# Kernel optimization log

Measured on AMD Instinct MI355X. Metric: run time of the kernel, lower is better.

## Reference

```python
import jax, jax.numpy as jnp
import numpy as np

B, T, I, H, O = 8192, 1024, 7, 100, 1


def setup_inputs() -> dict:
    key = jax.random.key(0)
    ks = jax.random.split(key, 7)
    s = 1.0 / np.sqrt(H)  # PyTorch default init bound for RNN/Linear(H)
    return {
        "x": jax.random.normal(ks[0], (B, T, I), dtype=jnp.float32),
        "W_ih": jax.random.uniform(ks[1], (H, I), jnp.float32, -s, s),
        "W_hh": jax.random.uniform(ks[2], (H, H), jnp.float32, -s, s),
        "b_ih": jax.random.uniform(ks[3], (H,), jnp.float32, -s, s),
        "b_hh": jax.random.uniform(ks[4], (H,), jnp.float32, -s, s),
        "W_fc": jax.random.uniform(ks[5], (O, H), jnp.float32, -s, s),
        "b_fc": jax.random.uniform(ks[6], (O,), jnp.float32, -s, s),
    }


def reference(x, W_ih, W_hh, b_ih, b_hh, W_fc, b_fc):
    # Precompute the input projection for all timesteps in one GEMM:
    # x_proj[b,t,h] = x[b,t,:] @ W_ih^T + b_ih + b_hh  (both biases folded in)
    x_proj = jnp.einsum('bti,hi->bth', x, W_ih) + b_ih + b_hh  # [B,T,H]

    def step(h, xt):
        # h_t = relu(x_t W_ih^T + b_ih + h_{t-1} W_hh^T + b_hh)
        h_new = jax.nn.relu(xt + h @ W_hh.T)
        return h_new, None

    h0 = jnp.zeros((x.shape[0], W_hh.shape[0]), dtype=x.dtype)  # [B,H]
    hT, _ = jax.lax.scan(step, h0, jnp.swapaxes(x_proj, 0, 1))  # scan over T

    # fc applied to last timestep only: out[:, -1, :] @ W_fc^T + b_fc
    return hT @ W_fc.T + b_fc  # [B,O]
```

## Files before the change

### kernel.cpp

```cpp
#include <hip/hip_runtime.h>


typedef _Float16 half8 __attribute__((ext_vector_type(8)));
typedef _Float16 half4 __attribute__((ext_vector_type(4)));
typedef float f32x4 __attribute__((ext_vector_type(4)));
typedef unsigned u32x4 __attribute__((ext_vector_type(4)));
typedef unsigned u32x2 __attribute__((ext_vector_type(2)));

static __device__ __forceinline__ unsigned pkrtz(float a, float b) {
    return __builtin_bit_cast(unsigned, __builtin_amdgcn_cvt_pkrtz(a, b));
}
static __device__ __forceinline__ f32x4 ld4(const float* p) {
    typedef f32x4 __attribute__((aligned(4))) f32x4a;
    return *(const f32x4a*)p;
}
static __device__ __forceinline__ u32x2 relu_pack(const f32x4 a) {
    u32x2 u = { pkrtz(a[0], a[1]), pkrtz(a[2], a[3]) };
    half4 h = __builtin_bit_cast(half4, u);
    const half4 z = { (_Float16)0, (_Float16)0, (_Float16)0, (_Float16)0 };
    h = __builtin_elementwise_max(h, z);
    return __builtin_bit_cast(u32x2, h);
}

#define MFMA16(a, b, c) __builtin_amdgcn_mfma_f32_16x16x32_f16(a, b, c, 0, 0, 0)

template<int NT, int TI0, int WID>
static __device__ __forceinline__ void rnn_half(
    const int l, const int lm, const int q, const bool q1,
    const float* __restrict__ x,
    const float* __restrict__ W_ih, const float* __restrict__ W_hh,
    const float* __restrict__ b_ih, const float* __restrict__ b_hh,
    const float* __restrict__ W_fc, const float* __restrict__ b_fc,
    float* __restrict__ out,
    u32x2 (*xch)[2][4][64], float* red)
{
    half8 w[NT][4];
#pragma unroll
    for (int i = 0; i < NT; ++i) {
        const int np = 16 * (TI0 + i) + lm;
#pragma unroll
        for (int kt = 0; kt < 4; ++kt) {
            half8 hw;
#pragma unroll
            for (int jj = 0; jj < 8; ++jj) {
                float v = 0.f;
                if (np < 100) {
                    if (jj < 4) {
                        int p = 16 * kt + 4 * q + jj;
                        if (p < 100) v = W_hh[np * 100 + p];
                    } else if (kt < 3) {
                        int p = 16 * (kt + 4) + 4 * q + (jj - 4);
                        if (p < 100) v = W_hh[np * 100 + p];
                    } else {
                        if (q == 0)      v = W_ih[np * 7 + (jj - 4)];
                        else if (q == 1) v = (jj < 7) ? W_ih[np * 7 + jj]
                                             : (b_ih[np] + b_hh[np]);
                    }
                }
                hw[jj] = (_Float16)v;
            }
            w[i][kt] = hw;
        }
    }

    const float* xr = x + (size_t)(blockIdx.x * 16 + lm) * 7168;
    const int xo = q1 ? 3 : 0;

    const u32x4 zz = {0u, 0u, 0u, 0u};
    const half8 hz = __builtin_bit_cast(half8, zz);

    half8 hf[4];
    {
        f32x4 v = ld4(xr + xo);
        float x0 = q1 ? v.y : v.x, x1 = q1 ? v.z : v.y;
        float x2 = q1 ? v.w : v.z, x3 = q1 ? 1.0f : v.w;
        hf[0] = hz; hf[1] = hz; hf[2] = hz;
        u32x4 h3 = {0u, 0u, pkrtz(x0, x1), pkrtz(x2, x3)};
        hf[3] = __builtin_bit_cast(half8, h3);
    }

    f32x4 xv[4];
#pragma unroll
    for (int s = 1; s <= 4; ++s) xv[s & 3] = ld4(xr + s * 7 + xo);

    const f32x4 kZ = {0.f, 0.f, 0.f, 0.f};
    f32x4 acc[NT];
#pragma unroll
    for (int i = 0; i < NT; ++i) acc[i] = kZ;

    for (int tb = 0; tb < 1024; tb += 4) {
#pragma unroll
        for (int u = 0; u < 4; ++u) {
            const int t = tb + u;
            const int p = u & 1;

#pragma unroll
            for (int kt = 0; kt < 4; ++kt)
#pragma unroll
                for (int i = 0; i < NT; ++i)
                    acc[i] = MFMA16(w[i][kt], hf[kt], kt == 0 ? kZ : acc[i]);

            u32x2 own[NT];
#pragma unroll
            for (int i = 0; i < NT; ++i) {
                own[i] = relu_pack(acc[i]);
                xch[p][WID][i][l] = own[i];
            }

            asm volatile("s_waitcnt lgkmcnt(0)" ::: "memory");
            __builtin_amdgcn_s_barrier();
            asm volatile("" ::: "memory");

            constexpr int NR = 7 - NT;
            u32x2 rd[NR];
#pragma unroll
            for (int j = 0; j < NR; ++j) rd[j] = xch[p][WID ^ 1][j][l];

            const int s = (u + 1) & 3;
            unsigned xd0, xd1;
            {
                f32x4 v = xv[s];
                float a_ = q1 ? v.y : v.x, b_ = q1 ? v.z : v.y;
                float c_ = q1 ? v.w : v.z, e_ = q1 ? 1.0f : v.w;
                xd0 = pkrtz(a_, b_); xd1 = pkrtz(c_, e_);
            }
            {
                int tn = t + 5; if (tn > 1023) tn = 1023;
                xv[s] = ld4(xr + tn * 7 + xo);
            }

#pragma unroll
            for (int kt = 0; kt < 3; ++kt) {
                u32x2 lo, hi;
                if constexpr (WID == 0) { lo = own[kt]; hi = rd[kt]; }
                else                    { lo = rd[kt];  hi = own[kt]; }
                u32x4 d = { lo.x, lo.y, hi.x, hi.y };
                hf[kt] = __builtin_bit_cast(half8, d);
            }
            {
                u32x2 lo;
                if constexpr (WID == 0) lo = own[3]; else lo = rd[3];
                u32x4 d = { lo.x, lo.y, xd0, xd1 };
                hf[3] = __builtin_bit_cast(half8, d);
            }
        }
    }

    float sum = 0.f;
#pragma unroll
    for (int i = 0; i < NT; ++i)
#pragma unroll
        for (int r = 0; r < 4; ++r) {
            const int np = 16 * (TI0 + i) + 4 * q + r;
            const float wf = (np < 100) ? W_fc[np] : 0.f;
            sum += wf * fmaxf(acc[i][r], 0.f);
        }
    if constexpr (WID == 1) red[l] = sum;
    asm volatile("s_waitcnt lgkmcnt(0)" ::: "memory");
    __builtin_amdgcn_s_barrier();
    asm volatile("" ::: "memory");
    if constexpr (WID == 0) {
        float s2 = sum + red[l];
        s2 += __shfl_xor(s2, 16, 64);
        s2 += __shfl_xor(s2, 32, 64);
        if (q == 0) out[blockIdx.x * 16 + lm] = s2 + b_fc[0];
    }
}

__global__ __launch_bounds__(128, 1)
void rnn_wave(const float* __restrict__ x,
              const float* __restrict__ W_ih,
              const float* __restrict__ W_hh,
              const float* __restrict__ b_ih,
              const float* __restrict__ b_hh,
              const float* __restrict__ W_fc,
              const float* __restrict__ b_fc,
              float* __restrict__ out) {
    __shared__ u32x2 xch[2][2][4][64];
    __shared__ float red[64];

    const int l  = threadIdx.x & 63;
    const int wv = threadIdx.x >> 6;
    const int lm = l & 15;
    const int q  = l >> 4;
    const bool q1 = (q == 1);

    if (wv == 0)
        rnn_half<4, 0, 0>(l, lm, q, q1, x, W_ih, W_hh, b_ih, b_hh, W_fc, b_fc,
                          out, xch, red);
    else
        rnn_half<3, 4, 1>(l, lm, q, q1, x, W_ih, W_hh, b_ih, b_hh, W_fc, b_fc,
                          out, xch, red);
}

extern "C" void kernel_launch(void* const* d_in, const int* in_sizes, int n_in,
                              void* d_out, int out_size, void* d_ws, size_t ws_size,
                              hipStream_t stream) {
    const float* x    = (const float*)d_in[0];
    const float* W_ih = (const float*)d_in[1];
    const float* W_hh = (const float*)d_in[2];
    const float* b_ih = (const float*)d_in[3];
    const float* b_hh = (const float*)d_in[4];
    const float* W_fc = (const float*)d_in[5];
    const float* b_fc = (const float*)d_in[6];
    float* out = (float*)d_out;

    rnn_wave<<<dim3(512), dim3(128), 0, stream>>>(x, W_ih, W_hh, b_ih, b_hh, W_fc, b_fc, out);
}
```

Before: 665.4 us.

## Remap hidden tiles so each wave starts MFMAs on its own output before the exchange

Reassigns output tiles across the two waves so that each wave's own previous outputs form complete K-slices. Each wave can then issue the first half of its MFMA chain before it needs the peer's data from LDS. The exchange now moves full 128-bit vectors of packed fp16 per lane, and stores are issued as soon as each pair of accumulators is ready. This is meant to overlap LDS traffic and barrier latency with matrix work on the serial recurrence. In exchange the tile mapping and the x-injection logic become more intricate, and the manual 4x unroll is removed.

```diff
diff --git a/kernel.cpp b/kernel.cpp
--- a/kernel.cpp
+++ b/kernel.cpp
@@ -2,10 +2,8 @@
 
 
 typedef _Float16 half8 __attribute__((ext_vector_type(8)));
-typedef _Float16 half4 __attribute__((ext_vector_type(4)));
 typedef float f32x4 __attribute__((ext_vector_type(4)));
 typedef unsigned u32x4 __attribute__((ext_vector_type(4)));
-typedef unsigned u32x2 __attribute__((ext_vector_type(2)));
 
 static __device__ __forceinline__ unsigned pkrtz(float a, float b) {
     return __builtin_bit_cast(unsigned, __builtin_amdgcn_cvt_pkrtz(a, b));
@@ -14,17 +12,22 @@
     typedef f32x4 __attribute__((aligned(4))) f32x4a;
     return *(const f32x4a*)p;
 }
-static __device__ __forceinline__ u32x2 relu_pack(const f32x4 a) {
-    u32x2 u = { pkrtz(a[0], a[1]), pkrtz(a[2], a[3]) };
-    half4 h = __builtin_bit_cast(half4, u);
-    const half4 z = { (_Float16)0, (_Float16)0, (_Float16)0, (_Float16)0 };
-    h = __builtin_elementwise_max(h, z);
-    return __builtin_bit_cast(u32x2, h);
+static __device__ __forceinline__ u32x4 pack_relu4(f32x4 a, f32x4 b) {
+    u32x4 u = { pkrtz(a[0], a[1]), pkrtz(a[2], a[3]),
+                pkrtz(b[0], b[1]), pkrtz(b[2], b[3]) };
+    const u32x4 zz = {0u, 0u, 0u, 0u};
+    half8 h = __builtin_elementwise_max(__builtin_bit_cast(half8, u),
+                                        __builtin_bit_cast(half8, zz));
+    return __builtin_bit_cast(u32x4, h);
 }
 
 #define MFMA16(a, b, c) __builtin_amdgcn_mfma_f32_16x16x32_f16(a, b, c, 0, 0, 0)
-
-template<int NT, int TI0, int WID>
+#define LGKM0() asm volatile("s_waitcnt lgkmcnt(0)" ::: "memory")
+#define FENCE() asm volatile("" ::: "memory")
+
+__constant__ int kTI[2][4] = {{0, 4, 1, 5}, {2, 6, 3, 0}};
+
+template<int WID>
 static __device__ __forceinline__ void rnn_half(
     const int l, const int lm, const int q, const bool q1,
     const float* __restrict__ x,
@@ -32,12 +35,16 @@
     const float* __restrict__ b_ih, const float* __restrict__ b_hh,
     const float* __restrict__ W_fc, const float* __restrict__ b_fc,
     float* __restrict__ out,
-    u32x2 (*xch)[2][4][64], float* red)
+    u32x4 (*xch)[4][64], float* red)
 {
+    constexpr int NT = (WID == 0) ? 4 : 3;
+
     half8 w[NT][4];
 #pragma unroll
     for (int i = 0; i < NT; ++i) {
-        const int np = 16 * (TI0 + i) + lm;
+        const int ti = (WID == 0) ? ((i & 1) * 4 + (i >> 1))
+                                  : (i == 0 ? 2 : (i == 1 ? 6 : 3));
+        const int np = 16 * ti + lm;
 #pragma unroll
         for (int kt = 0; kt < 4; ++kt) {
             half8 hw;
@@ -63,102 +70,123 @@
         }
     }
 
+    const u32x4 zz = {0u, 0u, 0u, 0u};
+    const f32x4 kZ = {0.f, 0.f, 0.f, 0.f};
+
     const float* xr = x + (size_t)(blockIdx.x * 16 + lm) * 7168;
     const int xo = q1 ? 3 : 0;
-
-    const u32x4 zz = {0u, 0u, 0u, 0u};
-    const half8 hz = __builtin_bit_cast(half8, zz);
-
-    half8 hf[4];
+    f32x4 xv[4];
+    if constexpr (WID == 1) {
+#pragma unroll
+        for (int s = 1; s <= 4; ++s) xv[s & 3] = ld4(xr + s * 7 + xo);
+    }
+
+    half8 hfA, hfB;
+    u32x4 rdA, rdB;
     {
-        f32x4 v = ld4(xr + xo);
-        float x0 = q1 ? v.y : v.x, x1 = q1 ? v.z : v.y;
-        float x2 = q1 ? v.w : v.z, x3 = q1 ? 1.0f : v.w;
-        hf[0] = hz; hf[1] = hz; hf[2] = hz;
-        u32x4 h3 = {0u, 0u, pkrtz(x0, x1), pkrtz(x2, x3)};
-        hf[3] = __builtin_bit_cast(half8, h3);
-    }
-
-    f32x4 xv[4];
-#pragma unroll
-    for (int s = 1; s <= 4; ++s) xv[s & 3] = ld4(xr + s * 7 + xo);
-
-    const f32x4 kZ = {0.f, 0.f, 0.f, 0.f};
+        u32x4 d0 = zz, d1 = zz;
+        if constexpr (WID == 1) {
+            f32x4 v = ld4(xr + xo);
+            float a_ = q1 ? v.y : v.x, b_ = q1 ? v.z : v.y;
+            float c_ = q1 ? v.w : v.z, e_ = q1 ? 1.0f : v.w;
+            d1.z = pkrtz(a_, b_); d1.w = pkrtz(c_, e_);
+        }
+        hfA = __builtin_bit_cast(half8, d0);
+        hfB = __builtin_bit_cast(half8, d1);
+        xch[0][WID * 2 + 0][l] = d0;
+        xch[0][WID * 2 + 1][l] = d1;
+        LGKM0();
+        __builtin_amdgcn_s_barrier();
+        FENCE();
+        rdA = xch[0][(WID ^ 1) * 2 + 0][l];
+        rdB = xch[0][(WID ^ 1) * 2 + 1][l];
+    }
+
     f32x4 acc[NT];
-#pragma unroll
-    for (int i = 0; i < NT; ++i) acc[i] = kZ;
-
-    for (int tb = 0; tb < 1024; tb += 4) {
-#pragma unroll
-        for (int u = 0; u < 4; ++u) {
-            const int t = tb + u;
-            const int p = u & 1;
-
-#pragma unroll
-            for (int kt = 0; kt < 4; ++kt)
-#pragma unroll
-                for (int i = 0; i < NT; ++i)
-                    acc[i] = MFMA16(w[i][kt], hf[kt], kt == 0 ? kZ : acc[i]);
-
-            u32x2 own[NT];
-#pragma unroll
-            for (int i = 0; i < NT; ++i) {
-                own[i] = relu_pack(acc[i]);
-                xch[p][WID][i][l] = own[i];
-            }
-
-            asm volatile("s_waitcnt lgkmcnt(0)" ::: "memory");
-            __builtin_amdgcn_s_barrier();
-            asm volatile("" ::: "memory");
-
-            constexpr int NR = 7 - NT;
-            u32x2 rd[NR];
-#pragma unroll
-            for (int j = 0; j < NR; ++j) rd[j] = xch[p][WID ^ 1][j][l];
-
-            const int s = (u + 1) & 3;
-            unsigned xd0, xd1;
-            {
-                f32x4 v = xv[s];
-                float a_ = q1 ? v.y : v.x, b_ = q1 ? v.z : v.y;
-                float c_ = q1 ? v.w : v.z, e_ = q1 ? 1.0f : v.w;
-                xd0 = pkrtz(a_, b_); xd1 = pkrtz(c_, e_);
-            }
-            {
-                int tn = t + 5; if (tn > 1023) tn = 1023;
-                xv[s] = ld4(xr + tn * 7 + xo);
-            }
-
-#pragma unroll
-            for (int kt = 0; kt < 3; ++kt) {
-                u32x2 lo, hi;
-                if constexpr (WID == 0) { lo = own[kt]; hi = rd[kt]; }
-                else                    { lo = rd[kt];  hi = own[kt]; }
-                u32x4 d = { lo.x, lo.y, hi.x, hi.y };
-                hf[kt] = __builtin_bit_cast(half8, d);
-            }
-            {
-                u32x2 lo;
-                if constexpr (WID == 0) lo = own[3]; else lo = rd[3];
-                u32x4 d = { lo.x, lo.y, xd0, xd1 };
-                hf[3] = __builtin_bit_cast(half8, d);
-            }
-        }
+
+    for (int t = 0; t < 1024; ++t) {
+        const int pn = (t + 1) & 1;
+
+        const half8 hp0 = __builtin_bit_cast(half8, rdA);
+        const half8 hp1 = __builtin_bit_cast(half8, rdB);
+
+        if constexpr (WID == 0) {
+            acc[0] = MFMA16(w[0][0], hfA, kZ);
+            acc[1] = MFMA16(w[1][0], hfA, kZ);
+            acc[2] = MFMA16(w[2][0], hfA, kZ);
+            acc[3] = MFMA16(w[3][0], hfA, kZ);
+            acc[0] = MFMA16(w[0][1], hfB, acc[0]);
+            acc[1] = MFMA16(w[1][1], hfB, acc[1]);
+            acc[2] = MFMA16(w[2][1], hfB, acc[2]);
+            acc[3] = MFMA16(w[3][1], hfB, acc[3]);
+            acc[0] = MFMA16(w[0][2], hp0, acc[0]);
+            acc[1] = MFMA16(w[1][2], hp0, acc[1]);
+            acc[2] = MFMA16(w[2][2], hp0, acc[2]);
+            acc[3] = MFMA16(w[3][2], hp0, acc[3]);
+            acc[0] = MFMA16(w[0][3], hp1, acc[0]);
+            acc[1] = MFMA16(w[1][3], hp1, acc[1]);
+            u32x4 d0 = pack_relu4(acc[0], acc[1]);
+            xch[pn][0][l] = d0;
+            acc[2] = MFMA16(w[2][3], hp1, acc[2]);
+            acc[3] = MFMA16(w[3][3], hp1, acc[3]);
+            u32x4 d1 = pack_relu4(acc[2], acc[3]);
+            xch[pn][1][l] = d1;
+            hfA = __builtin_bit_cast(half8, d0);
+            hfB = __builtin_bit_cast(half8, d1);
+        } else {
+            acc[0] = MFMA16(w[0][2], hfA, kZ);
+            acc[1] = MFMA16(w[1][2], hfA, kZ);
+            acc[2] = MFMA16(w[2][2], hfA, kZ);
+            acc[0] = MFMA16(w[0][3], hfB, acc[0]);
+            acc[1] = MFMA16(w[1][3], hfB, acc[1]);
+            acc[2] = MFMA16(w[2][3], hfB, acc[2]);
+            acc[0] = MFMA16(w[0][0], hp0, acc[0]);
+            acc[1] = MFMA16(w[1][0], hp0, acc[1]);
+            acc[2] = MFMA16(w[2][0], hp0, acc[2]);
+            acc[0] = MFMA16(w[0][1], hp1, acc[0]);
+            acc[1] = MFMA16(w[1][1], hp1, acc[1]);
+            u32x4 d2 = pack_relu4(acc[0], acc[1]);
+            xch[pn][2][l] = d2;
+            acc[2] = MFMA16(w[2][1], hp1, acc[2]);
+            const int s = (t + 1) & 3;
+            f32x4 v = xv[s];
+            float a_ = q1 ? v.y : v.x, b_ = q1 ? v.z : v.y;
+            float c_ = q1 ? v.w : v.z, e_ = q1 ? 1.0f : v.w;
+            u32x4 d3;
+            d3.x = pkrtz(fmaxf(acc[2][0], 0.f), fmaxf(acc[2][1], 0.f));
+            d3.y = pkrtz(fmaxf(acc[2][2], 0.f), fmaxf(acc[2][3], 0.f));
+            d3.z = pkrtz(a_, b_);
+            d3.w = pkrtz(c_, e_);
+            xch[pn][3][l] = d3;
+            int tn = t + 5; if (tn > 1023) tn = 1023;
+            xv[s] = ld4(xr + tn * 7 + xo);
+            hfA = __builtin_bit_cast(half8, d2);
+            hfB = __builtin_bit_cast(half8, d3);
+        }
+
+        LGKM0();
+        __builtin_amdgcn_s_barrier();
+        FENCE();
+        rdA = xch[pn][(WID ^ 1) * 2 + 0][l];
+        rdB = xch[pn][(WID ^ 1) * 2 + 1][l];
     }
 
     float sum = 0.f;
 #pragma unroll
-    for (int i = 0; i < NT; ++i)
+    for (int i = 0; i < NT; ++i) {
+        const int ti = (WID == 0) ? ((i & 1) * 4 + (i >> 1))
+                                  : (i == 0 ? 2 : (i == 1 ? 6 : 3));
 #pragma unroll
         for (int r = 0; r < 4; ++r) {
-            const int np = 16 * (TI0 + i) + 4 * q + r;
+            const int np = 16 * ti + 4 * q + r;
             const float wf = (np < 100) ? W_fc[np] : 0.f;
             sum += wf * fmaxf(acc[i][r], 0.f);
         }
+    }
     if constexpr (WID == 1) red[l] = sum;
-    asm volatile("s_waitcnt lgkmcnt(0)" ::: "memory");
+    LGKM0();
     __builtin_amdgcn_s_barrier();
-    asm volatile("" ::: "memory");
+    FENCE();
     if constexpr (WID == 0) {
         float s2 = sum + red[l];
         s2 += __shfl_xor(s2, 16, 64);
@@ -176,7 +204,7 @@
               const float* __restrict__ W_fc,
               const float* __restrict__ b_fc,
               float* __restrict__ out) {
-    __shared__ u32x2 xch[2][2][4][64];
+    __shared__ u32x4 xch[2][4][64];
     __shared__ float red[64];
 
     const int l  = threadIdx.x & 63;
@@ -186,11 +214,11 @@
     const bool q1 = (q == 1);
 
     if (wv == 0)
-        rnn_half<4, 0, 0>(l, lm, q, q1, x, W_ih, W_hh, b_ih, b_hh, W_fc, b_fc,
-                          out, xch, red);
+        rnn_half<0>(l, lm, q, q1, x, W_ih, W_hh, b_ih, b_hh, W_fc, b_fc,
+                    out, xch, red);
     else
-        rnn_half<3, 4, 1>(l, lm, q, q1, x, W_ih, W_hh, b_ih, b_hh, W_fc, b_fc,
-                          out, xch, red);
+        rnn_half<1>(l, lm, q, q1, x, W_ih, W_hh, b_ih, b_hh, W_fc, b_fc,
+                    out, xch, red);
 }
 
 extern "C" void kernel_launch(void* const* d_in, const int* in_sizes, int n_in,
```

Result: slower. 747.2 us (+12.3%).
